# Kernel optimization log

Measured on AMD Instinct MI355X. Metric: run time of the kernel, lower is better.

## Reference

```python
import jax, jax.numpy as jnp
import numpy as np

N = 10000
E = 160000
D_IN = 512
D_HID = 512


def gcn_conv(x, W, b, src, dst, norm, num_nodes):
    # x: [N, Fin] -> h: [N, Fout]; PyG GCNConv: linear transform, then
    # symmetric-normalized aggregation over edges with self-loops.
    h = x @ W + b  # [N, Fout]
    msgs = h[src] * norm[:, None]  # [E', Fout]
    return jax.ops.segment_sum(msgs, dst, num_segments=num_nodes)


def _norm_with_self_loops(edge_index, num_nodes):
    loop = jnp.arange(num_nodes, dtype=edge_index.dtype)
    src = jnp.concatenate([edge_index[0], loop])
    dst = jnp.concatenate([edge_index[1], loop])
    deg = jax.ops.segment_sum(jnp.ones_like(dst, dtype=jnp.float32), dst,
                              num_segments=num_nodes)
    dis = jnp.where(deg > 0, jax.lax.rsqrt(jnp.maximum(deg, 1.0)), 0.0)
    norm = dis[src] * dis[dst]
    return src, dst, norm


def setup_inputs() -> dict:
    key = jax.random.key(0)
    ks = jax.random.split(key, 8)
    x = jax.random.normal(ks[0], (N, D_IN), dtype=jnp.float32)
    edge_index = jax.random.randint(ks[1], (2, E), 0, N, dtype=jnp.int64)
    s1 = 1.0 / np.sqrt(D_IN)
    s2 = 1.0 / np.sqrt(D_HID)
    W1 = jax.random.uniform(ks[2], (D_IN, D_HID), jnp.float32, -s1, s1)
    b1 = jnp.zeros((D_HID,), jnp.float32)
    W2 = jax.random.uniform(ks[3], (D_HID, D_IN), jnp.float32, -s2, s2)
    b2 = jnp.zeros((D_IN,), jnp.float32)
    Wp1 = jax.random.uniform(ks[4], (D_HID, D_HID), jnp.float32, -s2, s2)
    bp1 = jnp.zeros((D_HID,), jnp.float32)
    Wp2 = jax.random.uniform(ks[5], (D_HID, D_HID), jnp.float32, -s2, s2)
    bp2 = jnp.zeros((D_HID,), jnp.float32)
    return {"x": x, "edge_index": edge_index, "W1": W1, "b1": b1,
            "W2": W2, "b2": b2, "Wp1": Wp1, "bp1": bp1,
            "Wp2": Wp2, "bp2": bp2}


def reference(x, edge_index, W1, b1, W2, b2, Wp1, bp1, Wp2, bp2):
    num_nodes = x.shape[0]
    src, dst, norm = _norm_with_self_loops(edge_index, num_nodes)
    z = gcn_conv(x, W1, b1, src, dst, norm, num_nodes)        # [N, hidden]
    h = jax.nn.relu(z)
    out = gcn_conv(h, W2, b2, src, dst, norm, num_nodes)      # [N, in]
    proj = jax.nn.relu(z @ Wp1 + bp1) @ Wp2 + bp2             # [N, hidden]
    return (out, z, proj)
```

## Files before the change

### kernel.cpp

```cpp
#include <hip/hip_runtime.h>
#include <stddef.h>

#define N_NODES 10000
#define N_EDGES 160000
#define DIM     512
#define RBT     158
#define RB128   79
#define GBLKS   (RB128 * 4)
#define SCAN_BLKS 40
#define EBLKS   625

typedef short bf16x8 __attribute__((ext_vector_type(8)));
typedef float f32x4  __attribute__((ext_vector_type(4)));

__device__ inline unsigned short bf16_rne(float f) {
    unsigned u = __builtin_bit_cast(unsigned, f);
    u += 0x7FFF + ((u >> 16) & 1);
    return (unsigned short)(u >> 16);
}
__device__ inline float bf16_to_f32(unsigned short h) {
    unsigned u = ((unsigned)h) << 16;
    return __builtin_bit_cast(float, u);
}

__device__ inline void gld_lds16(const void* g, void* lds) {
    __builtin_amdgcn_global_load_lds(
        (const __attribute__((address_space(1))) void*)g,
        (__attribute__((address_space(3))) void*)lds, 16, 0, 0);
}


__global__ __launch_bounds__(256) void packw_zero_kernel(
    const float* __restrict__ W1, const float* __restrict__ W2,
    const float* __restrict__ Wp1, const float* __restrict__ Wp2,
    short* __restrict__ T1, short* __restrict__ T2,
    short* __restrict__ Tp1, short* __restrict__ Tp2,
    int* __restrict__ deg) {
    const int bid = blockIdx.x;
    if (bid >= 512) {
        int i = (bid - 512) * 256 + threadIdx.x;
        if (i < N_NODES) deg[i] = 0;
        return;
    }
    const int wsel = bid >> 7;
    const float* W = (wsel == 0) ? W1 : (wsel == 1) ? W2 : (wsel == 2) ? Wp1 : Wp2;
    short* WT      = (wsel == 0) ? T1 : (wsel == 1) ? T2 : (wsel == 2) ? Tp1 : Tp2;
    int id = (bid & 127) * 256 + threadIdx.x;
    int n  = id & 511;
    int kc = id >> 9;
    int colblk = n >> 6, col = n & 63;
    int kt = kc >> 2, kq = kc & 3;
    short hi[8];
#pragma unroll
    for (int j = 0; j < 8; ++j)
        hi[j] = (short)bf16_rne(W[(size_t)(kc * 8 + j) * 512 + n]);
    size_t base = (size_t)(colblk * 16 + kt) * 2048 + col * 32 + ((kq ^ ((col >> 1) & 3)) << 3);
    *(int4*)(WT + base) = *(const int4*)hi;
}


__global__ __launch_bounds__(256) void packa_count_kernel(
    const float* __restrict__ A, short* __restrict__ P0,
    const int* __restrict__ ei, int* __restrict__ deg) {
    const int bid = blockIdx.x;
    if (bid >= RBT * 16) {
        int e = (bid - RBT * 16) * 256 + threadIdx.x;
        if (e < N_EDGES) atomicAdd(&deg[ei[N_EDGES + e]], 1);
        return;
    }
    const int kt = bid & 15;
    const int rb = bid >> 4;
    const int t  = threadIdx.x;
    const int r  = t >> 2;
    const int kq = t & 3;
    const int row = rb * 64 + r;
    float v[8] = {};
    if (row < N_NODES) {
        float4 a = *(const float4*)(A + (size_t)row * 512 + kt * 32 + kq * 8);
        float4 b = *(const float4*)(A + (size_t)row * 512 + kt * 32 + kq * 8 + 4);
        v[0]=a.x; v[1]=a.y; v[2]=a.z; v[3]=a.w; v[4]=b.x; v[5]=b.y; v[6]=b.z; v[7]=b.w;
    }
    short hi[8];
#pragma unroll
    for (int j = 0; j < 8; ++j) hi[j] = (short)bf16_rne(v[j]);
    size_t base = (size_t)(rb * 16 + kt) * 2048 + r * 32 + ((kq ^ ((r >> 1) & 3)) << 3);
    *(int4*)(P0 + base) = *(const int4*)hi;
}


__global__ __launch_bounds__(256) void scan1_kernel(const int* __restrict__ deg,
                                                    int* __restrict__ row_off,
                                                    int* __restrict__ bsum,
                                                    float* __restrict__ dis,
                                                    int* __restrict__ cursor, int n) {
    __shared__ int sm[256];
    const int i = blockIdx.x * 256 + threadIdx.x;
    int v = (i < n) ? deg[i] : 0;
    if (i < n) {
        dis[i] = rsqrtf((float)(v + 1));
        cursor[i] = 0;
    }
    sm[threadIdx.x] = v;
    __syncthreads();
    for (int off = 1; off < 256; off <<= 1) {
        int t = (threadIdx.x >= (unsigned)off) ? sm[threadIdx.x - off] : 0;
        __syncthreads();
        sm[threadIdx.x] += t;
        __syncthreads();
    }
    if (i < n) row_off[i + 1] = sm[threadIdx.x];
    if (threadIdx.x == 255) bsum[blockIdx.x] = sm[255];
}

__global__ __launch_bounds__(64) void scan2_kernel(int* __restrict__ bsum) {
    const int lane = threadIdx.x;
    int v0 = (lane < SCAN_BLKS) ? bsum[lane] : 0;
    int v = v0;
    for (int off = 1; off < 64; off <<= 1) {
        int t = __shfl_up(v, off, 64);
        if (lane >= off) v += t;
    }
    if (lane < SCAN_BLKS) bsum[lane] = v - v0;
}

__global__ __launch_bounds__(256) void scan3_kernel(int* __restrict__ row_off,
                                                    const int* __restrict__ bsum, int n) {
    const int i = blockIdx.x * 256 + threadIdx.x;
    if (i < n) row_off[i + 1] += bsum[blockIdx.x];
    if (i == 0) row_off[0] = 0;
}


__device__ __forceinline__ void map_block(int bid, int& rb, int& cb) {
    const int q = GBLKS / 8;
    const int r = GBLKS % 8;
    int xcd = bid & 7;
    int idx = bid >> 3;
    int L = (xcd < r ? xcd * (q + 1) : r * (q + 1) + (xcd - r) * q) + idx;
    cb = L / RB128;
    rb = L - cb * RB128;
}

__device__ __forceinline__ void gemm128_core(
    const short* __restrict__ Apk, const short* __restrict__ Wpk,
    int bid, f32x4 (&acc)[4][4],
    short (*As)[4096], short (*Bs)[4096],
    int& rb, int& cb, int& wr, int& wc)
{
    map_block(bid, rb, cb);
    const int tid = threadIdx.x;
    const int w = tid >> 6;
    wr = w >> 1;
    wc = w & 1;
    const int lane = tid & 63;
    const int l15 = lane & 15, kg = lane >> 4;
    const int kso = ((kg ^ ((l15 >> 1) & 3)) << 3);
    const int wofs = w * 1024;

    const char* At0 = (const char*)(Apk + (size_t)(rb * 2)     * 16 * 2048);
    const char* At1 = (const char*)(Apk + (size_t)(rb * 2 + 1) * 16 * 2048);
    const char* Bt0 = (const char*)(Wpk + (size_t)(cb * 2)     * 16 * 2048);
    const char* Bt1 = (const char*)(Wpk + (size_t)(cb * 2 + 1) * 16 * 2048);

#pragma unroll
    for (int i = 0; i < 4; ++i)
#pragma unroll
        for (int j = 0; j < 4; ++j) acc[i][j] = (f32x4){0.f, 0.f, 0.f, 0.f};

    auto stage = [&](int buf, int kt) {
        const int go = kt * 4096 + tid * 16;
        char* ad = (char*)&As[buf][0];
        char* bd = (char*)&Bs[buf][0];
        gld_lds16(At0 + go, ad + wofs);
        gld_lds16(At1 + go, ad + 4096 + wofs);
        gld_lds16(Bt0 + go, bd + wofs);
        gld_lds16(Bt1 + go, bd + 4096 + wofs);
    };

    stage(0, 0);
    stage(1, 1);

#pragma unroll
    for (int kt = 0; kt < 16; ++kt) {
        const int buf = kt % 3;
        if (kt < 15) {
            asm volatile("s_waitcnt vmcnt(4)" ::: "memory");
        } else {
            asm volatile("s_waitcnt vmcnt(0)" ::: "memory");
        }
        __builtin_amdgcn_s_barrier();
        __builtin_amdgcn_sched_barrier(0);
        if (kt < 14) stage((kt + 2) % 3, kt + 2);

        const short* as = &As[buf][wr * 2048];
        const short* bs = &Bs[buf][wc * 2048];
        bf16x8 af[4], bf[4];
#pragma unroll
        for (int m = 0; m < 4; ++m)
            af[m] = *(const bf16x8*)&as[(m * 16 + l15) * 32 + kso];
#pragma unroll
        for (int n = 0; n < 4; ++n)
            bf[n] = *(const bf16x8*)&bs[(n * 16 + l15) * 32 + kso];
#pragma unroll
        for (int m = 0; m < 4; ++m)
#pragma unroll
            for (int n = 0; n < 4; ++n)
                acc[m][n] = __builtin_amdgcn_mfma_f32_16x16x32_bf16(af[m], bf[n], acc[m][n], 0, 0, 0);
    }
}


template<bool RELU_OUT>
__device__ __forceinline__ void epi128_f32(f32x4 (&acc)[4][4], const float* bias,
                                           float* C, int rb, int cb, int wr, int wc) {
    const int lane = threadIdx.x & 63;
    const int l15 = lane & 15, kg = lane >> 4;
#pragma unroll
    for (int n = 0; n < 4; ++n) {
        int c = cb * 128 + wc * 64 + n * 16 + l15;
        float bv = bias[c];
#pragma unroll
        for (int m = 0; m < 4; ++m) {
            int r0 = rb * 128 + wr * 64 + m * 16 + kg * 4;
#pragma unroll
            for (int j = 0; j < 4; ++j) {
                int row = r0 + j;
                if (row < N_NODES) {
                    float v = acc[m][n][j] + bv;
                    if (RELU_OUT) v = fmaxf(v, 0.f);
                    C[(size_t)row * 512 + c] = v;
                }
            }
        }
    }
}

__device__ __forceinline__ void epi128_bf16(f32x4 (&acc)[4][4], const float* bias,
                                            unsigned short* C, int rb, int cb, int wr, int wc) {
    const int lane = threadIdx.x & 63;
    const int l15 = lane & 15, kg = lane >> 4;
#pragma unroll
    for (int n = 0; n < 4; ++n) {
        int c = cb * 128 + wc * 64 + n * 16 + l15;
        float bv = bias[c];
#pragma unroll
        for (int m = 0; m < 4; ++m) {
            int r0 = rb * 128 + wr * 64 + m * 16 + kg * 4;
#pragma unroll
            for (int j = 0; j < 4; ++j) {
                int row = r0 + j;
                if (row < N_NODES)
                    C[(size_t)row * 512 + c] = bf16_rne(acc[m][n][j] + bv);
            }
        }
    }
}

__device__ __forceinline__ void epi128_pack(f32x4 (&acc)[4][4], const float* bias,
                                            short* Cpk, int rb, int cb, int wr, int wc) {
    const int lane = threadIdx.x & 63;
    const int l15 = lane & 15, kg = lane >> 4;
#pragma unroll
    for (int n = 0; n < 4; ++n) {
        int c = cb * 128 + wc * 64 + n * 16 + l15;
        int kt_n = c >> 5, kk = c & 31, kgn = kk >> 3, kj = kk & 7;
        float bv = bias[c];
#pragma unroll
        for (int m = 0; m < 4; ++m) {
#pragma unroll
            for (int j = 0; j < 4; ++j) {
                int grow = rb * 128 + wr * 64 + m * 16 + kg * 4 + j;
                float v = (grow < N_NODES) ? fmaxf(acc[m][n][j] + bv, 0.f) : 0.f;
                int rt = grow >> 6, rl = grow & 63;
                size_t dst = (size_t)(rt * 16 + kt_n) * 2048 + rl * 32
                           + ((kgn ^ ((rl >> 1) & 3)) << 3) + kj;
                Cpk[dst] = (short)bf16_rne(v);
            }
        }
    }
}


__global__ __launch_bounds__(256, 3) void gemm1_scatter_kernel(
    const short* __restrict__ APKx, const short* __restrict__ WT1,
    const float* __restrict__ b1, unsigned short* __restrict__ Hb,
    const int* __restrict__ ei, const float* __restrict__ dis,
    const int* __restrict__ row_off, int* __restrict__ cursor,
    int* __restrict__ csr_src, float* __restrict__ csr_norm)
{
    __shared__ short As[3][4096];
    __shared__ short Bs[3][4096];
    const int bid = blockIdx.x;
    if (bid >= GBLKS) {
        int e = (bid - GBLKS) * 256 + threadIdx.x;
        if (e < N_EDGES) {
            int s = ei[e];
            int d = ei[N_EDGES + e];
            int slot = row_off[d] + atomicAdd(&cursor[d], 1);
            csr_src[slot]  = s;
            csr_norm[slot] = dis[s] * dis[d];
        }
        return;
    }
    f32x4 acc[4][4];
    int rb, cb, wr, wc;
    gemm128_core(APKx, WT1, bid, acc, As, Bs, rb, cb, wr, wc);
    epi128_bf16(acc, b1, Hb, rb, cb, wr, wc);
}


__global__ __launch_bounds__(256) void agg1_pack_kernel(
    const unsigned short* __restrict__ Hb,
    const float* __restrict__ dis,
    const int* __restrict__ row_off,
    const int* __restrict__ csr_src,
    const float* __restrict__ csr_norm,
    float* __restrict__ z,
    short* __restrict__ ZPKp, short* __restrict__ ZPKr)
{
    const int node = blockIdx.x;
    const int t = threadIdx.x;
    const int f0 = 2 * t;
    const int kt = f0 >> 5, kq = (f0 >> 3) & 3, j = f0 & 7;
    const int rb = node >> 6, r = node & 63;
    const size_t dst = (size_t)(rb * 16 + kt) * 2048 + r * 32 + ((kq ^ ((r >> 1) & 3)) << 3) + j;

    if (node >= N_NODES) {
        ushort2 zz = make_ushort2(0, 0);
        *(ushort2*)(ZPKp + dst) = zz;
        *(ushort2*)(ZPKr + dst) = zz;
        return;
    }

    const int start = row_off[node];
    const int end   = row_off[node + 1];
    const float dn = dis[node];
    const float sw = dn * dn;

    ushort2 hv = *((const ushort2*)(Hb + (size_t)node * DIM) + t);
    float a0 = bf16_to_f32(hv.x) * sw;
    float a1 = bf16_to_f32(hv.y) * sw;

    int e = start;
    for (; e + 3 < end; e += 4) {
        int s0 = csr_src[e],     s1 = csr_src[e + 1];
        int s2 = csr_src[e + 2], s3 = csr_src[e + 3];
        float w0 = csr_norm[e],     w1 = csr_norm[e + 1];
        float w2 = csr_norm[e + 2], w3 = csr_norm[e + 3];
        ushort2 v0 = *((const ushort2*)(Hb + (size_t)s0 * DIM) + t);
        ushort2 v1 = *((const ushort2*)(Hb + (size_t)s1 * DIM) + t);
        ushort2 v2 = *((const ushort2*)(Hb + (size_t)s2 * DIM) + t);
        ushort2 v3 = *((const ushort2*)(Hb + (size_t)s3 * DIM) + t);
        a0 += bf16_to_f32(v0.x) * w0 + bf16_to_f32(v1.x) * w1
            + bf16_to_f32(v2.x) * w2 + bf16_to_f32(v3.x) * w3;
        a1 += bf16_to_f32(v0.y) * w0 + bf16_to_f32(v1.y) * w1
            + bf16_to_f32(v2.y) * w2 + bf16_to_f32(v3.y) * w3;
    }
    for (; e < end; ++e) {
        int s = csr_src[e];
        float w = csr_norm[e];
        ushort2 v = *((const ushort2*)(Hb + (size_t)s * DIM) + t);
        a0 += bf16_to_f32(v.x) * w;
        a1 += bf16_to_f32(v.y) * w;
    }
    *((float2*)(z + (size_t)node * DIM) + t) = make_float2(a0, a1);

    *(ushort2*)(ZPKp + dst) = make_ushort2(bf16_rne(a0), bf16_rne(a1));
    *(ushort2*)(ZPKr + dst) = make_ushort2(bf16_rne(fmaxf(a0, 0.f)), bf16_rne(fmaxf(a1, 0.f)));
}


__global__ __launch_bounds__(256, 3) void gemm23_kernel(
    const short* __restrict__ ZPKr, const short* __restrict__ WT2,
    const float* __restrict__ b2, unsigned short* __restrict__ Hb,
    const short* __restrict__ ZPKp, const short* __restrict__ WTp1,
    const float* __restrict__ bp1, short* __restrict__ APKp1)
{
    __shared__ short As[3][4096];
    __shared__ short Bs[3][4096];
    const int bid = blockIdx.x;
    f32x4 acc[4][4];
    int rb, cb, wr, wc;
    if (bid < GBLKS) {
        gemm128_core(ZPKr, WT2, bid, acc, As, Bs, rb, cb, wr, wc);
        epi128_bf16(acc, b2, Hb, rb, cb, wr, wc);
    } else {
        gemm128_core(ZPKp, WTp1, bid - GBLKS, acc, As, Bs, rb, cb, wr, wc);
        epi128_pack(acc, bp1, APKp1, rb, cb, wr, wc);
    }
}


__global__ __launch_bounds__(256) void agg2_kernel(
    const unsigned short* __restrict__ Hb, const float* __restrict__ dis,
    const int* __restrict__ row_off, const int* __restrict__ csr_src,
    const float* __restrict__ csr_norm, float* __restrict__ out)
{
    const int node = blockIdx.x;
    const int t = threadIdx.x;
    const int start = row_off[node];
    const int end   = row_off[node + 1];
    const float dn = dis[node];
    const float sw = dn * dn;

    ushort2 hv = *((const ushort2*)(Hb + (size_t)node * DIM) + t);
    float a0 = bf16_to_f32(hv.x) * sw;
    float a1 = bf16_to_f32(hv.y) * sw;

    int e = start;
    for (; e + 3 < end; e += 4) {
        int s0 = csr_src[e],     s1 = csr_src[e + 1];
        int s2 = csr_src[e + 2], s3 = csr_src[e + 3];
        float w0 = csr_norm[e],     w1 = csr_norm[e + 1];
        float w2 = csr_norm[e + 2], w3 = csr_norm[e + 3];
        ushort2 v0 = *((const ushort2*)(Hb + (size_t)s0 * DIM) + t);
        ushort2 v1 = *((const ushort2*)(Hb + (size_t)s1 * DIM) + t);
        ushort2 v2 = *((const ushort2*)(Hb + (size_t)s2 * DIM) + t);
        ushort2 v3 = *((const ushort2*)(Hb + (size_t)s3 * DIM) + t);
        a0 += bf16_to_f32(v0.x) * w0 + bf16_to_f32(v1.x) * w1
            + bf16_to_f32(v2.x) * w2 + bf16_to_f32(v3.x) * w3;
        a1 += bf16_to_f32(v0.y) * w0 + bf16_to_f32(v1.y) * w1
            + bf16_to_f32(v2.y) * w2 + bf16_to_f32(v3.y) * w3;
    }
    for (; e < end; ++e) {
        int s = csr_src[e];
        float w = csr_norm[e];
        ushort2 v = *((const ushort2*)(Hb + (size_t)s * DIM) + t);
        a0 += bf16_to_f32(v.x) * w;
        a1 += bf16_to_f32(v.y) * w;
    }
    *((float2*)(out + (size_t)node * DIM) + t) = make_float2(a0, a1);
}


__global__ __launch_bounds__(256, 3) void gemm4_kernel(
    const short* __restrict__ APKp1, const short* __restrict__ WTp2,
    const float* __restrict__ bp2, float* __restrict__ proj)
{
    __shared__ short As[3][4096];
    __shared__ short Bs[3][4096];
    f32x4 acc[4][4];
    int rb, cb, wr, wc;
    gemm128_core(APKp1, WTp2, blockIdx.x, acc, As, Bs, rb, cb, wr, wc);
    epi128_f32<false>(acc, bp2, proj, rb, cb, wr, wc);
}


extern "C" void kernel_launch(void* const* d_in, const int* in_sizes, int n_in,
                              void* d_out, int out_size, void* d_ws, size_t ws_size,
                              hipStream_t stream) {
    const float* x   = (const float*)d_in[0];
    const int*   ei  = (const int*)d_in[1];
    const float* W1  = (const float*)d_in[2];
    const float* b1  = (const float*)d_in[3];
    const float* W2  = (const float*)d_in[4];
    const float* b2  = (const float*)d_in[5];
    const float* Wp1 = (const float*)d_in[6];
    const float* bp1 = (const float*)d_in[7];
    const float* Wp2 = (const float*)d_in[8];
    const float* bp2 = (const float*)d_in[9];

    float* out  = (float*)d_out;
    float* z    = out + (size_t)N_NODES * DIM;
    float* proj = z   + (size_t)N_NODES * DIM;

    char* ws = (char*)d_ws;
    size_t off = 0;
    auto walloc = [&](size_t bytes) -> void* {
        void* p = ws + off;
        off = (off + bytes + 255) & ~(size_t)255;
        return p;
    };
    const size_t PK_SHORTS = (size_t)RBT * 16 * 2048;
    unsigned short* Hb = (unsigned short*)walloc((size_t)N_NODES * DIM * sizeof(unsigned short));
    short* APKx  = (short*)walloc(PK_SHORTS * sizeof(short));
    short* ZPKp  = (short*)walloc(PK_SHORTS * sizeof(short));
    short* ZPKr  = (short*)walloc(PK_SHORTS * sizeof(short));
    short* APKp1 = (short*)walloc(PK_SHORTS * sizeof(short));
    short* WT1  = (short*)walloc((size_t)8 * 16 * 2048 * sizeof(short));
    short* WT2  = (short*)walloc((size_t)8 * 16 * 2048 * sizeof(short));
    short* WTp1 = (short*)walloc((size_t)8 * 16 * 2048 * sizeof(short));
    short* WTp2 = (short*)walloc((size_t)8 * 16 * 2048 * sizeof(short));
    int*   deg      = (int*)  walloc(N_NODES * sizeof(int));
    int*   cursor   = (int*)  walloc(N_NODES * sizeof(int));
    int*   row_off  = (int*)  walloc((N_NODES + 1) * sizeof(int));
    int*   bsum     = (int*)  walloc(SCAN_BLKS * sizeof(int));
    float* dis      = (float*)walloc(N_NODES * sizeof(float));
    int*   csr_src  = (int*)  walloc(N_EDGES * sizeof(int));
    float* csr_norm = (float*)walloc(N_EDGES * sizeof(float));

    const dim3 blk(256);
    const dim3 wave(64);

    packw_zero_kernel<<<dim3(512 + SCAN_BLKS), blk, 0, stream>>>(
        W1, W2, Wp1, Wp2, WT1, WT2, WTp1, WTp2, deg);
    packa_count_kernel<<<dim3(RBT * 16 + EBLKS), blk, 0, stream>>>(x, APKx, ei, deg);
    scan1_kernel<<<dim3(SCAN_BLKS), blk, 0, stream>>>(deg, row_off, bsum, dis, cursor, N_NODES);
    scan2_kernel<<<dim3(1), wave, 0, stream>>>(bsum);
    scan3_kernel<<<dim3(SCAN_BLKS), blk, 0, stream>>>(row_off, bsum, N_NODES);

    gemm1_scatter_kernel<<<dim3(GBLKS + EBLKS), blk, 0, stream>>>(
        APKx, WT1, b1, Hb, ei, dis, row_off, cursor, csr_src, csr_norm);
    agg1_pack_kernel<<<dim3(RB128 * 128), blk, 0, stream>>>(
        Hb, dis, row_off, csr_src, csr_norm, z, ZPKp, ZPKr);
    gemm23_kernel<<<dim3(2 * GBLKS), blk, 0, stream>>>(
        ZPKr, WT2, b2, Hb, ZPKp, WTp1, bp1, APKp1);
    agg2_kernel<<<dim3(N_NODES), blk, 0, stream>>>(Hb, dis, row_off, csr_src, csr_norm, out);
    gemm4_kernel<<<dim3(GBLKS), blk, 0, stream>>>(APKp1, WTp2, bp2, proj);
}
```

Measured before the change: 155.6 us.

## Merge prep kernels, apply ReLU in GEMM A-load, widen aggregation unroll, remap tiles

```diff
diff --git a/kernel.cpp b/kernel.cpp
--- a/kernel.cpp
+++ b/kernel.cpp
@@ -9,6 +9,7 @@
 #define GBLKS   (RB128 * 4)
 #define SCAN_BLKS 40
 #define EBLKS   625
+#define PAKBLKS (RBT * 16)
 
 typedef short bf16x8 __attribute__((ext_vector_type(8)));
 typedef float f32x4  __attribute__((ext_vector_type(4)));
@@ -29,62 +30,61 @@
         (__attribute__((address_space(3))) void*)lds, 16, 0, 0);
 }
 
-
-__global__ __launch_bounds__(256) void packw_zero_kernel(
+__device__ __forceinline__ bf16x8 relu_pk(bf16x8 v) {
+    bf16x8 r;
+#pragma unroll
+    for (int i = 0; i < 8; ++i) r[i] = (v[i] < (short)0) ? (short)0 : v[i];
+    return r;
+}
+
+
+__global__ __launch_bounds__(256) void prep_kernel(
     const float* __restrict__ W1, const float* __restrict__ W2,
     const float* __restrict__ Wp1, const float* __restrict__ Wp2,
     short* __restrict__ T1, short* __restrict__ T2,
     short* __restrict__ Tp1, short* __restrict__ Tp2,
-    int* __restrict__ deg) {
+    const float* __restrict__ X, short* __restrict__ APKx,
+    const int* __restrict__ ei, int* __restrict__ deg)
+{
     const int bid = blockIdx.x;
-    if (bid >= 512) {
-        int i = (bid - 512) * 256 + threadIdx.x;
-        if (i < N_NODES) deg[i] = 0;
-        return;
-    }
-    const int wsel = bid >> 7;
-    const float* W = (wsel == 0) ? W1 : (wsel == 1) ? W2 : (wsel == 2) ? Wp1 : Wp2;
-    short* WT      = (wsel == 0) ? T1 : (wsel == 1) ? T2 : (wsel == 2) ? Tp1 : Tp2;
-    int id = (bid & 127) * 256 + threadIdx.x;
-    int n  = id & 511;
-    int kc = id >> 9;
-    int colblk = n >> 6, col = n & 63;
-    int kt = kc >> 2, kq = kc & 3;
-    short hi[8];
-#pragma unroll
-    for (int j = 0; j < 8; ++j)
-        hi[j] = (short)bf16_rne(W[(size_t)(kc * 8 + j) * 512 + n]);
-    size_t base = (size_t)(colblk * 16 + kt) * 2048 + col * 32 + ((kq ^ ((col >> 1) & 3)) << 3);
-    *(int4*)(WT + base) = *(const int4*)hi;
-}
-
-
-__global__ __launch_bounds__(256) void packa_count_kernel(
-    const float* __restrict__ A, short* __restrict__ P0,
-    const int* __restrict__ ei, int* __restrict__ deg) {
-    const int bid = blockIdx.x;
-    if (bid >= RBT * 16) {
-        int e = (bid - RBT * 16) * 256 + threadIdx.x;
+    if (bid < 512) {
+        const int wsel = bid >> 7;
+        const float* W = (wsel == 0) ? W1 : (wsel == 1) ? W2 : (wsel == 2) ? Wp1 : Wp2;
+        short* WT      = (wsel == 0) ? T1 : (wsel == 1) ? T2 : (wsel == 2) ? Tp1 : Tp2;
+        int id = (bid & 127) * 256 + threadIdx.x;
+        int n  = id & 511;
+        int kc = id >> 9;
+        int colblk = n >> 6, col = n & 63;
+        int kt = kc >> 2, kq = kc & 3;
+        short hi[8];
+#pragma unroll
+        for (int j = 0; j < 8; ++j)
+            hi[j] = (short)bf16_rne(W[(size_t)(kc * 8 + j) * 512 + n]);
+        size_t base = (size_t)(colblk * 16 + kt) * 2048 + col * 32 + ((kq ^ ((col >> 1) & 3)) << 3);
+        *(int4*)(WT + base) = *(const int4*)hi;
+    } else if (bid < 512 + PAKBLKS) {
+        const int pb = bid - 512;
+        const int kt = pb & 15;
+        const int rb = pb >> 4;
+        const int t  = threadIdx.x;
+        const int r  = t >> 2;
+        const int kq = t & 3;
+        const int row = rb * 64 + r;
+        float v[8] = {};
+        if (row < N_NODES) {
+            float4 a = *(const float4*)(X + (size_t)row * 512 + kt * 32 + kq * 8);
+            float4 b = *(const float4*)(X + (size_t)row * 512 + kt * 32 + kq * 8 + 4);
+            v[0]=a.x; v[1]=a.y; v[2]=a.z; v[3]=a.w; v[4]=b.x; v[5]=b.y; v[6]=b.z; v[7]=b.w;
+        }
+        short hi[8];
+#pragma unroll
+        for (int j = 0; j < 8; ++j) hi[j] = (short)bf16_rne(v[j]);
+        size_t base = (size_t)(rb * 16 + kt) * 2048 + r * 32 + ((kq ^ ((r >> 1) & 3)) << 3);
+        *(int4*)(APKx + base) = *(const int4*)hi;
+    } else {
+        int e = (bid - 512 - PAKBLKS) * 256 + threadIdx.x;
         if (e < N_EDGES) atomicAdd(&deg[ei[N_EDGES + e]], 1);
-        return;
-    }
-    const int kt = bid & 15;
-    const int rb = bid >> 4;
-    const int t  = threadIdx.x;
-    const int r  = t >> 2;
-    const int kq = t & 3;
-    const int row = rb * 64 + r;
-    float v[8] = {};
-    if (row < N_NODES) {
-        float4 a = *(const float4*)(A + (size_t)row * 512 + kt * 32 + kq * 8);
-        float4 b = *(const float4*)(A + (size_t)row * 512 + kt * 32 + kq * 8 + 4);
-        v[0]=a.x; v[1]=a.y; v[2]=a.z; v[3]=a.w; v[4]=b.x; v[5]=b.y; v[6]=b.z; v[7]=b.w;
-    }
-    short hi[8];
-#pragma unroll
-    for (int j = 0; j < 8; ++j) hi[j] = (short)bf16_rne(v[j]);
-    size_t base = (size_t)(rb * 16 + kt) * 2048 + r * 32 + ((kq ^ ((r >> 1) & 3)) << 3);
-    *(int4*)(P0 + base) = *(const int4*)hi;
+    }
 }
 
 
@@ -137,10 +137,11 @@
     int xcd = bid & 7;
     int idx = bid >> 3;
     int L = (xcd < r ? xcd * (q + 1) : r * (q + 1) + (xcd - r) * q) + idx;
-    cb = L / RB128;
-    rb = L - cb * RB128;
-}
-
+    rb = L >> 2;
+    cb = L & 3;
+}
+
+template<bool RELU_A>
 __device__ __forceinline__ void gemm128_core(
     const short* __restrict__ Apk, const short* __restrict__ Wpk,
     int bid, f32x4 (&acc)[4][4],
@@ -196,8 +197,10 @@
         const short* bs = &Bs[buf][wc * 2048];
         bf16x8 af[4], bf[4];
 #pragma unroll
-        for (int m = 0; m < 4; ++m)
+        for (int m = 0; m < 4; ++m) {
             af[m] = *(const bf16x8*)&as[(m * 16 + l15) * 32 + kso];
+            if (RELU_A) af[m] = relu_pk(af[m]);
+        }
 #pragma unroll
         for (int n = 0; n < 4; ++n)
             bf[n] = *(const bf16x8*)&bs[(n * 16 + l15) * 32 + kso];
@@ -304,7 +307,7 @@
     }
     f32x4 acc[4][4];
     int rb, cb, wr, wc;
-    gemm128_core(APKx, WT1, bid, acc, As, Bs, rb, cb, wr, wc);
+    gemm128_core<false>(APKx, WT1, bid, acc, As, Bs, rb, cb, wr, wc);
     epi128_bf16(acc, b1, Hb, rb, cb, wr, wc);
 }
 
@@ -316,7 +319,7 @@
     const int* __restrict__ csr_src,
     const float* __restrict__ csr_norm,
     float* __restrict__ z,
-    short* __restrict__ ZPKp, short* __restrict__ ZPKr)
+    short* __restrict__ ZPKp)
 {
     const int node = blockIdx.x;
     const int t = threadIdx.x;
@@ -326,9 +329,7 @@
     const size_t dst = (size_t)(rb * 16 + kt) * 2048 + r * 32 + ((kq ^ ((r >> 1) & 3)) << 3) + j;
 
     if (node >= N_NODES) {
-        ushort2 zz = make_ushort2(0, 0);
-        *(ushort2*)(ZPKp + dst) = zz;
-        *(ushort2*)(ZPKr + dst) = zz;
+        *(ushort2*)(ZPKp + dst) = make_ushort2(0, 0);
         return;
     }
 
@@ -342,38 +343,34 @@
     float a1 = bf16_to_f32(hv.y) * sw;
 
     int e = start;
-    for (; e + 3 < end; e += 4) {
-        int s0 = csr_src[e],     s1 = csr_src[e + 1];
-        int s2 = csr_src[e + 2], s3 = csr_src[e + 3];
-        float w0 = csr_norm[e],     w1 = csr_norm[e + 1];
-        float w2 = csr_norm[e + 2], w3 = csr_norm[e + 3];
-        ushort2 v0 = *((const ushort2*)(Hb + (size_t)s0 * DIM) + t);
-        ushort2 v1 = *((const ushort2*)(Hb + (size_t)s1 * DIM) + t);
-        ushort2 v2 = *((const ushort2*)(Hb + (size_t)s2 * DIM) + t);
-        ushort2 v3 = *((const ushort2*)(Hb + (size_t)s3 * DIM) + t);
-        a0 += bf16_to_f32(v0.x) * w0 + bf16_to_f32(v1.x) * w1
-            + bf16_to_f32(v2.x) * w2 + bf16_to_f32(v3.x) * w3;
-        a1 += bf16_to_f32(v0.y) * w0 + bf16_to_f32(v1.y) * w1
-            + bf16_to_f32(v2.y) * w2 + bf16_to_f32(v3.y) * w3;
+    for (; e + 7 < end; e += 8) {
+        int s[8]; float w[8]; ushort2 v[8];
+#pragma unroll
+        for (int i = 0; i < 8; ++i) { s[i] = csr_src[e + i]; w[i] = csr_norm[e + i]; }
+#pragma unroll
+        for (int i = 0; i < 8; ++i) v[i] = *((const ushort2*)(Hb + (size_t)s[i] * DIM) + t);
+#pragma unroll
+        for (int i = 0; i < 8; ++i) {
+            a0 += bf16_to_f32(v[i].x) * w[i];
+            a1 += bf16_to_f32(v[i].y) * w[i];
+        }
     }
     for (; e < end; ++e) {
-        int s = csr_src[e];
-        float w = csr_norm[e];
-        ushort2 v = *((const ushort2*)(Hb + (size_t)s * DIM) + t);
-        a0 += bf16_to_f32(v.x) * w;
-        a1 += bf16_to_f32(v.y) * w;
+        int si = csr_src[e];
+        float wi = csr_norm[e];
+        ushort2 vi = *((const ushort2*)(Hb + (size_t)si * DIM) + t);
+        a0 += bf16_to_f32(vi.x) * wi;
+        a1 += bf16_to_f32(vi.y) * wi;
     }
     *((float2*)(z + (size_t)node * DIM) + t) = make_float2(a0, a1);
-
     *(ushort2*)(ZPKp + dst) = make_ushort2(bf16_rne(a0), bf16_rne(a1));
-    *(ushort2*)(ZPKr + dst) = make_ushort2(bf16_rne(fmaxf(a0, 0.f)), bf16_rne(fmaxf(a1, 0.f)));
 }
 
 
 __global__ __launch_bounds__(256, 3) void gemm23_kernel(
-    const short* __restrict__ ZPKr, const short* __restrict__ WT2,
+    const short* __restrict__ ZPKp, const short* __restrict__ WT2,
     const float* __restrict__ b2, unsigned short* __restrict__ Hb,
-    const short* __restrict__ ZPKp, const short* __restrict__ WTp1,
+    const short* __restrict__ WTp1,
     const float* __restrict__ bp1, short* __restrict__ APKp1)
 {
     __shared__ short As[3][4096];
@@ -382,10 +379,10 @@
     f32x4 acc[4][4];
     int rb, cb, wr, wc;
     if (bid < GBLKS) {
-        gemm128_core(ZPKr, WT2, bid, acc, As, Bs, rb, cb, wr, wc);
+        gemm128_core<true>(ZPKp, WT2, bid, acc, As, Bs, rb, cb, wr, wc);
         epi128_bf16(acc, b2, Hb, rb, cb, wr, wc);
     } else {
-        gemm128_core(ZPKp, WTp1, bid - GBLKS, acc, As, Bs, rb, cb, wr, wc);
+        gemm128_core<false>(ZPKp, WTp1, bid - GBLKS, acc, As, Bs, rb, cb, wr, wc);
         epi128_pack(acc, bp1, APKp1, rb, cb, wr, wc);
     }
 }
@@ -408,26 +405,24 @@
     float a1 = bf16_to_f32(hv.y) * sw;
 
     int e = start;
-    for (; e + 3 < end; e += 4) {
-        int s0 = csr_src[e],     s1 = csr_src[e + 1];
-        int s2 = csr_src[e + 2], s3 = csr_src[e + 3];
-        float w0 = csr_norm[e],     w1 = csr_norm[e + 1];
-        float w2 = csr_norm[e + 2], w3 = csr_norm[e + 3];
-        ushort2 v0 = *((const ushort2*)(Hb + (size_t)s0 * DIM) + t);
-        ushort2 v1 = *((const ushort2*)(Hb + (size_t)s1 * DIM) + t);
-        ushort2 v2 = *((const ushort2*)(Hb + (size_t)s2 * DIM) + t);
-        ushort2 v3 = *((const ushort2*)(Hb + (size_t)s3 * DIM) + t);
-        a0 += bf16_to_f32(v0.x) * w0 + bf16_to_f32(v1.x) * w1
-            + bf16_to_f32(v2.x) * w2 + bf16_to_f32(v3.x) * w3;
-        a1 += bf16_to_f32(v0.y) * w0 + bf16_to_f32(v1.y) * w1
-            + bf16_to_f32(v2.y) * w2 + bf16_to_f32(v3.y) * w3;
+    for (; e + 7 < end; e += 8) {
+        int s[8]; float w[8]; ushort2 v[8];
+#pragma unroll
+        for (int i = 0; i < 8; ++i) { s[i] = csr_src[e + i]; w[i] = csr_norm[e + i]; }
+#pragma unroll
+        for (int i = 0; i < 8; ++i) v[i] = *((const ushort2*)(Hb + (size_t)s[i] * DIM) + t);
+#pragma unroll
+        for (int i = 0; i < 8; ++i) {
+            a0 += bf16_to_f32(v[i].x) * w[i];
+            a1 += bf16_to_f32(v[i].y) * w[i];
+        }
     }
     for (; e < end; ++e) {
-        int s = csr_src[e];
-        float w = csr_norm[e];
-        ushort2 v = *((const ushort2*)(Hb + (size_t)s * DIM) + t);
-        a0 += bf16_to_f32(v.x) * w;
-        a1 += bf16_to_f32(v.y) * w;
+        int si = csr_src[e];
+        float wi = csr_norm[e];
+        ushort2 vi = *((const ushort2*)(Hb + (size_t)si * DIM) + t);
+        a0 += bf16_to_f32(vi.x) * wi;
+        a1 += bf16_to_f32(vi.y) * wi;
     }
     *((float2*)(out + (size_t)node * DIM) + t) = make_float2(a0, a1);
 }
@@ -441,7 +436,7 @@
     __shared__ short Bs[3][4096];
     f32x4 acc[4][4];
     int rb, cb, wr, wc;
-    gemm128_core(APKp1, WTp2, blockIdx.x, acc, As, Bs, rb, cb, wr, wc);
+    gemm128_core<false>(APKp1, WTp2, blockIdx.x, acc, As, Bs, rb, cb, wr, wc);
     epi128_f32<false>(acc, bp2, proj, rb, cb, wr, wc);
 }
 
@@ -475,7 +470,6 @@
     unsigned short* Hb = (unsigned short*)walloc((size_t)N_NODES * DIM * sizeof(unsigned short));
     short* APKx  = (short*)walloc(PK_SHORTS * sizeof(short));
     short* ZPKp  = (short*)walloc(PK_SHORTS * sizeof(short));
-    short* ZPKr  = (short*)walloc(PK_SHORTS * sizeof(short));
     short* APKp1 = (short*)walloc(PK_SHORTS * sizeof(short));
     short* WT1  = (short*)walloc((size_t)8 * 16 * 2048 * sizeof(short));
     short* WT2  = (short*)walloc((size_t)8 * 16 * 2048 * sizeof(short));
@@ -492,9 +486,9 @@
     const dim3 blk(256);
     const dim3 wave(64);
 
-    packw_zero_kernel<<<dim3(512 + SCAN_BLKS), blk, 0, stream>>>(
-        W1, W2, Wp1, Wp2, WT1, WT2, WTp1, WTp2, deg);
-    packa_count_kernel<<<dim3(RBT * 16 + EBLKS), blk, 0, stream>>>(x, APKx, ei, deg);
+    hipMemsetAsync(deg, 0, N_NODES * sizeof(int), stream);
+    prep_kernel<<<dim3(512 + PAKBLKS + EBLKS), blk, 0, stream>>>(
+        W1, W2, Wp1, Wp2, WT1, WT2, WTp1, WTp2, x, APKx, ei, deg);
     scan1_kernel<<<dim3(SCAN_BLKS), blk, 0, stream>>>(deg, row_off, bsum, dis, cursor, N_NODES);
     scan2_kernel<<<dim3(1), wave, 0, stream>>>(bsum);
     scan3_kernel<<<dim3(SCAN_BLKS), blk, 0, stream>>>(row_off, bsum, N_NODES);
@@ -502,9 +496,9 @@
     gemm1_scatter_kernel<<<dim3(GBLKS + EBLKS), blk, 0, stream>>>(
         APKx, WT1, b1, Hb, ei, dis, row_off, cursor, csr_src, csr_norm);
     agg1_pack_kernel<<<dim3(RB128 * 128), blk, 0, stream>>>(
-        Hb, dis, row_off, csr_src, csr_norm, z, ZPKp, ZPKr);
+        Hb, dis, row_off, csr_src, csr_norm, z, ZPKp);
     gemm23_kernel<<<dim3(2 * GBLKS), blk, 0, stream>>>(
-        ZPKr, WT2, b2, Hb, ZPKp, WTp1, bp1, APKp1);
+        ZPKp, WT2, b2, Hb, WTp1, bp1, APKp1);
     agg2_kernel<<<dim3(N_NODES), blk, 0, stream>>>(Hb, dis, row_off, csr_src, csr_norm, out);
     gemm4_kernel<<<dim3(GBLKS), blk, 0, stream>>>(APKp1, WTp2, bp2, proj);
 }
```

Result: faster. 148.6 us (-4.5%).
